# Optimization experiments

Hardware: AMD Instinct MI355X
Metric: run time of the kernel (lower is better)

## Reference

```python
import jax, jax.numpy as jnp
import numpy as np

# SLAY feature-map hyperparams (must match init_kwargs)
H, D, P, M, R = 4, 128, 16, 32, 2   # heads, head_dim, poly_dim, num_features, quad nodes
EPS = 1e-6
C = 2.0 + EPS
_nodes, _weights = np.polynomial.laguerre.laggauss(R)
QUAD_NODES = jnp.asarray(_nodes, jnp.float32) / C
QUAD_WEIGHTS = jnp.asarray(_weights, jnp.float32) / C

VOCAB, NUM_LABELS, EMBED_DIM = 100000, 32768, 512
B, S, K = 512, 64, 5


def slay_features(x, omega, anchors):
    """SLAY feature map: tensor product of anchored polynomial and PRF features.
    x: [N, EMBED_DIM] -> [N, R*H*P*M]"""
    N = x.shape[0]
    xr = x.reshape(N, H, D)
    xn = xr / jnp.clip(jnp.linalg.norm(xr, axis=-1, keepdims=True), 1e-6)  # safe_normalize
    # anchored polynomial features: [N, H, P]
    poly_feat = jnp.einsum('nhd,pd->nhp', xn, anchors) ** 2 / jnp.sqrt(float(P))
    # positive random features with Gauss-Laguerre quadrature: [R, N, H, M]
    prf_proj = jnp.einsum('nhd,rhdm->rnhm', xn, omega)
    s = QUAD_NODES.reshape(R, 1, 1, 1)
    sqrt_2s = jnp.sqrt(2.0 * jnp.clip(s, 0))
    prf_feat = jnp.exp(jnp.clip(prf_proj * sqrt_2s - s, -10.0, 10.0)) / jnp.sqrt(float(M))
    prf_feat = prf_feat * jnp.sqrt(jnp.clip(QUAD_WEIGHTS.reshape(R, 1, 1, 1), 0))
    # tensor-product fusion: [N, R, H, P, M] -> [N, R*H*P*M]
    fused = jnp.einsum('nhp,rnhm->nrhpm', poly_feat, prf_feat)
    return fused.reshape(N, -1)


def mean_embedding(indices, mask, embedding_table):
    embeds = embedding_table[indices]                       # [B, S, E]
    sum_embeds = jnp.sum(embeds * mask[:, :, None], axis=1)  # [B, E]
    sum_mask = jnp.sum(mask, axis=1, keepdims=True)
    return sum_embeds / jnp.clip(sum_mask, 1e-9)


def setup_inputs() -> dict:
    key = jax.random.key(0)
    k1, k2, k3, k4, k5, k6 = jax.random.split(key, 6)
    indices = jax.random.randint(k1, (B, S), 0, VOCAB)
    mask = jnp.ones((B, S), dtype=jnp.float32)
    labels = jax.random.randint(k2, (B, K), 0, NUM_LABELS)
    label_mask = jnp.ones((B, K), dtype=jnp.float32)
    embedding_table = jax.random.normal(k3, (VOCAB, EMBED_DIM), dtype=jnp.float32) * 0.02
    classifier_kernel = jax.random.normal(k4, (EMBED_DIM, NUM_LABELS), dtype=jnp.float32) * 0.02
    omega = jax.random.normal(k5, (R, H, D, M), dtype=jnp.float32)
    anchors = jax.random.normal(k6, (P, D), dtype=jnp.float32)
    anchors = anchors / jnp.linalg.norm(anchors, axis=-1, keepdims=True)
    return {"indices": indices, "mask": mask, "labels": labels, "label_mask": label_mask,
            "embedding_table": embedding_table, "classifier_kernel": classifier_kernel,
            "omega": omega, "anchors": anchors}


def reference(indices, mask, labels, label_mask, embedding_table, classifier_kernel, omega, anchors):
    query = mean_embedding(indices, mask, embedding_table)            # [B, E]
    phi_query = slay_features(query, omega, anchors)                  # [B, F]
    W_vecs = classifier_kernel.T                                      # [L, E]
    phi_W = slay_features(W_vecs, omega, anchors)                     # [L, F]  (dominant cost)
    Z_approx_vec = jnp.sum(phi_W, axis=0)                             # [F]
    denom = jnp.dot(phi_query, Z_approx_vec) + 1e-6                   # [B]
    log_Z = jnp.log(denom)
    safe_labels = jnp.maximum(labels, 0)
    W_pos = W_vecs[safe_labels]                                       # [B, K, E]
    phi_w_pos = slay_features(W_pos.reshape(-1, EMBED_DIM), omega, anchors).reshape(B, K, -1)
    nums = jnp.sum(phi_w_pos * phi_query[:, None, :], axis=-1) + 1e-6  # [B, K]
    log_probs = jnp.log(nums) - log_Z[:, None]
    loss_total = -jnp.sum(log_probs * label_mask)
    return loss_total / B
```

## Files before the change

### kernel.cpp

```cpp
#include <hip/hip_runtime.h>
#include <math.h>


namespace {
constexpr double Cq  = 2.0 + 1e-6;
constexpr double QN0 = 0.5857864376269049  / Cq;
constexpr double QN1 = 3.414213562373095   / Cq;
constexpr double QW0 = 0.8535533905932738  / Cq;
constexpr double QW1 = 0.14644660940672624 / Cq;

constexpr size_t OFF_POLYQ = 0;
constexpr size_t OFF_PRFQ  = 32768;
constexpr size_t OFF_Z     = OFF_PRFQ + 131072;
constexpr size_t OFF_ANCT  = OFF_Z + 4096;
constexpr size_t OFF_SLOT  = OFF_ANCT + 2048;
constexpr size_t OFF_FEAT  = OFF_SLOT + 32768;
constexpr size_t OFF_WPACK = OFF_FEAT + 819200;
constexpr size_t OFF_ZPART = OFF_WPACK + 43008;
}

__global__ void k_setup_a(const float* __restrict__ anchors,
                          const float* __restrict__ omega,
                          int* __restrict__ slot, float* __restrict__ Z,
                          float* __restrict__ out, float* __restrict__ anct,
                          float* __restrict__ Wpack)
{
    int t = blockIdx.x * 256 + threadIdx.x;
    for (int i = t; i < 32768; i += 16384) slot[i] = -1;
    if (t < 4096) Z[t] = 0.f;
    if (t == 0) out[0] = 0.f;
    if (t < 2048) {
        int p = t & 15, d = t >> 4;
        anct[t] = anchors[p * 128 + d];
    }
    for (int i = t; i < 4 * 128 * 84; i += 16384) {
        int o = i % 84, hd = i / 84, d = hd & 127, h = hd >> 7;
        float v = 0.f;
        if (o < 16) v = anchors[o * 128 + d];
        else if (o < 80) {
            int r = (o - 16) >> 5, m = (o - 16) & 31;
            v = omega[(((r * 4 + h) * 128) + d) * 32 + m];
        }
        Wpack[i] = v;
    }
}

__global__ void k_setup_b(const int* __restrict__ labels, int* __restrict__ slot)
{
    int i = blockIdx.x * 256 + threadIdx.x;
    if (i < 2560) slot[max(labels[i], 0)] = i;
}

__global__ void __launch_bounds__(256) k_embed_feat(const int* __restrict__ idx,
        const float* __restrict__ mask, const float* __restrict__ emb,
        const float* __restrict__ anct, const float* __restrict__ omega,
        float* __restrict__ polyq, float* __restrict__ prfq)
{
    __shared__ float xs[512];
    __shared__ float rnS[4];
    int b = blockIdx.x, t = threadIdx.x;

    float2 acc = make_float2(0.f, 0.f);
    float msum = 0.f;
#pragma unroll 8
    for (int s = 0; s < 64; ++s) {
        float mv = mask[b * 64 + s];
        const float2* row = (const float2*)(emb + (size_t)idx[b * 64 + s] * 512);
        float2 v = row[t];
        acc.x = fmaf(mv, v.x, acc.x);
        acc.y = fmaf(mv, v.y, acc.y);
        msum += mv;
    }
    float inv = 1.0f / fmaxf(msum, 1e-9f);
    xs[2 * t]     = acc.x * inv;
    xs[2 * t + 1] = acc.y * inv;
    __syncthreads();

    int w = t >> 6, lane = t & 63;
    {
        float v0 = xs[w * 128 + lane], v1 = xs[w * 128 + 64 + lane];
        float ss = fmaf(v0, v0, v1 * v1);
#pragma unroll
        for (int o = 1; o < 64; o <<= 1) ss += __shfl_xor(ss, o, 64);
        if (lane == 0) rnS[w] = 1.0f / fmaxf(sqrtf(ss), 1e-6f);
    }
    __syncthreads();

    const float s_[2] = {(float)QN0, (float)QN1};
    const float g_[2] = {sqrtf(2.0f * (float)QN0), sqrtf(2.0f * (float)QN1)};
    const float c_[2] = {sqrtf((float)QW0) * 0.17677669529663687f,
                         sqrtf((float)QW1) * 0.17677669529663687f};

    for (int tau = t; tau < 320; tau += 256) {
        int h = tau / 80, j = tau - h * 80;
        const float* xh = xs + h * 128;
        float a = 0.f;
        if (j < 16) {
            for (int d = 0; d < 128; ++d) a = fmaf(xh[d], anct[d * 16 + j], a);
            float v = a * rnS[h];
            polyq[(b * 4 + h) * 16 + j] = v * v * 0.25f;
        } else {
            int rj = j - 16, r = rj >> 5, m = rj & 31;
            const float* om = omega + ((size_t)(r * 4 + h) * 128) * 32 + m;
            for (int d = 0; d < 128; ++d) a = fmaf(xh[d], om[d * 32], a);
            float z = a * rnS[h] * g_[r] - s_[r];
            z = fminf(fmaxf(z, -10.f), 10.f);
            prfq[((b * 2 + r) * 4 + h) * 32 + m] = expf(z) * c_[r];
        }
    }
}

__global__ void __launch_bounds__(256) k_labels(const float* __restrict__ ck,
                                                const float* __restrict__ Wpack,
                                                const int* __restrict__ slot,
                                                float* __restrict__ feat,
                                                float* __restrict__ Zpart)
{
    __shared__ float xs[8192];
    __shared__ int slS[64];
    float* ex = xs;

    int t = threadIdx.x, w = t >> 6, lane = t & 63;
    int bid = blockIdx.x;
    int g = bid >> 2, h = bid & 3;
    int l0 = g * 64;

    if (t < 64) slS[t] = slot[l0 + t];

    {
        const float* src = ck + (size_t)h * 128 * 32768 + l0;
#pragma unroll
        for (int k = 0; k < 32; ++k) {
            int idx = k * 256 + t;
            int d = idx >> 6, lab = idx & 63;
            xs[idx] = src[(size_t)d * 32768 + lab];
        }
    }
    __syncthreads();

    int o0u = __builtin_amdgcn_readfirstlane(w * 21);
    const float* wrow = Wpack + (size_t)h * 128 * 84 + o0u;
    float acc[21] = {};
    float sumsq = 0.f;
    for (int d = 0; d < 128; ++d) {
        float xv = xs[d * 64 + lane];
        sumsq = fmaf(xv, xv, sumsq);
        const float* c = wrow + d * 84;
#pragma unroll
        for (int i = 0; i < 21; ++i) acc[i] = fmaf(xv, c[i], acc[i]);
    }
    __syncthreads();

#pragma unroll
    for (int i = 0; i < 21; ++i) {
        int o = o0u + i;
        if (o < 80) ex[lane * 85 + o] = acc[i];
    }
    if (w == 3) ex[lane * 85 + 80] = sumsq;
    __syncthreads();

    {
        int l = t & 63, part = t >> 6, o0 = part * 20;
        float rn = 1.0f / fmaxf(sqrtf(ex[l * 85 + 80]), 1e-6f);
        const float s_[2] = {(float)QN0, (float)QN1};
        const float g_[2] = {sqrtf(2.0f * (float)QN0), sqrtf(2.0f * (float)QN1)};
        const float c_[2] = {sqrtf((float)QW0) * 0.17677669529663687f,
                             sqrtf((float)QW1) * 0.17677669529663687f};
#pragma unroll
        for (int i = 0; i < 20; ++i) {
            int o = o0 + i;
            float v = ex[l * 85 + o];
            if (o < 16) {
                v = v * rn;
                v = v * v * 0.25f;
            } else {
                int r = (o - 16) >> 5;
                float z = v * rn * g_[r] - s_[r];
                z = fminf(fmaxf(z, -10.f), 10.f);
                v = expf(z) * c_[r];
            }
            ex[l * 85 + o] = v;
        }
    }
    __syncthreads();

    for (int j = 0; j < 64; ++j) {
        int s = slS[j];
        if (s >= 0 && t < 80)
            feat[((size_t)s * 4 + h) * 80 + t] = ex[j * 85 + t];
    }

    if (t < 128) {
        int r = t >> 6, p0 = ((t >> 3) & 7) * 2, m0 = (t & 7) * 4;
        float z0[4] = {}, z1[4] = {};
        for (int j = 0; j < 64; ++j) {
            const float* row = ex + j * 85;
            float pa = row[p0], pb = row[p0 + 1];
            const float* pf = row + 16 + r * 32 + m0;
#pragma unroll
            for (int k = 0; k < 4; ++k) {
                float fv = pf[k];
                z0[k] = fmaf(pa, fv, z0[k]);
                z1[k] = fmaf(pb, fv, z1[k]);
            }
        }
        float* zp = Zpart + (size_t)bid * 1024;
#pragma unroll
        for (int k = 0; k < 4; ++k) {
            zp[(r * 16 + p0) * 32 + m0 + k]     = z0[k];
            zp[(r * 16 + p0 + 1) * 32 + m0 + k] = z1[k];
        }
    }
}

__global__ void k_zreduce(const float* __restrict__ Zpart, float* __restrict__ Z)
{
    int tid = blockIdx.x * 256 + threadIdx.x;
    int e = tid & 1023, h = (tid >> 10) & 3, chunk = tid >> 12;
    float sum = 0.f;
    int g0 = chunk * 64;
#pragma unroll 4
    for (int g = g0; g < g0 + 64; ++g)
        sum += Zpart[(size_t)((g << 2) | h) * 1024 + e];
    atomicAdd(&Z[(e >> 9) * 2048 + h * 512 + (e & 511)], sum);
}

__global__ void k_final(const float* __restrict__ polyq, const float* __restrict__ prfq,
                        const float* __restrict__ Z, const int* __restrict__ labels,
                        const float* __restrict__ lmask, const int* __restrict__ slot,
                        const float* __restrict__ feat, float* __restrict__ out)
{
    int t = threadIdx.x, lane = t & 63;
    int b = blockIdx.x * 4 + (t >> 6);

    float acc = 0.f;
    for (int i = 0; i < 64; ++i) {
        int f = i * 64 + lane;
        int m = f & 31, p = (f >> 5) & 15, hh = (f >> 9) & 3, r = f >> 11;
        float phi = polyq[(b * 4 + hh) * 16 + p] * prfq[((b * 2 + r) * 4 + hh) * 32 + m];
        acc = fmaf(phi, Z[f], acc);
    }
#pragma unroll
    for (int o = 1; o < 64; o <<= 1) acc += __shfl_xor(acc, o, 64);
    float logZb = logf(acc + 1e-6f);

    if (lane < 20) {
        int k = lane >> 2, h = lane & 3;
        int l = max(labels[b * 5 + k], 0);
        int s = slot[l];
        const float4* f4 = (const float4*)(feat + ((size_t)s * 4 + h) * 80);
        const float* pq = polyq + (b * 4 + h) * 16;
        const float* q0 = prfq + ((b * 2 + 0) * 4 + h) * 32;
        const float* q1 = prfq + ((b * 2 + 1) * 4 + h) * 32;

        float pd = 0.f;
#pragma unroll
        for (int j = 0; j < 4; ++j) {
            float4 fp = f4[j];
            pd = fmaf(fp.x, pq[4*j+0], pd);
            pd = fmaf(fp.y, pq[4*j+1], pd);
            pd = fmaf(fp.z, pq[4*j+2], pd);
            pd = fmaf(fp.w, pq[4*j+3], pd);
        }
        float f0 = 0.f, f1 = 0.f;
#pragma unroll
        for (int j = 0; j < 8; ++j) {
            float4 fv = f4[4 + j];
            f0 = fmaf(fv.x, q0[4*j+0], f0);
            f0 = fmaf(fv.y, q0[4*j+1], f0);
            f0 = fmaf(fv.z, q0[4*j+2], f0);
            f0 = fmaf(fv.w, q0[4*j+3], f0);
            float4 fw = f4[12 + j];
            f1 = fmaf(fw.x, q1[4*j+0], f1);
            f1 = fmaf(fw.y, q1[4*j+1], f1);
            f1 = fmaf(fw.z, q1[4*j+2], f1);
            f1 = fmaf(fw.w, q1[4*j+3], f1);
        }
        float c = pd * (f0 + f1);
        c += __shfl_xor(c, 1, 64);
        c += __shfl_xor(c, 2, 64);
        if (h == 0) {
            float val = (logf(c + 1e-6f) - logZb) * lmask[b * 5 + k];
            atomicAdd(out, val * (-1.0f / 512.0f));
        }
    }
}

extern "C" void kernel_launch(void* const* d_in, const int* in_sizes, int n_in,
                              void* d_out, int out_size, void* d_ws, size_t ws_size,
                              hipStream_t stream)
{
    const int*   indices = (const int*)  d_in[0];
    const float* mask    = (const float*)d_in[1];
    const int*   labels  = (const int*)  d_in[2];
    const float* lmask   = (const float*)d_in[3];
    const float* emb     = (const float*)d_in[4];
    const float* ck      = (const float*)d_in[5];
    const float* omega   = (const float*)d_in[6];
    const float* anchors = (const float*)d_in[7];
    float* ws  = (float*)d_ws;
    float* out = (float*)d_out;
    int*   slot = (int*)(ws + OFF_SLOT);

    k_setup_a<<<64, 256, 0, stream>>>(anchors, omega, slot, ws + OFF_Z, out,
                                      ws + OFF_ANCT, ws + OFF_WPACK);
    k_setup_b<<<10, 256, 0, stream>>>(labels, slot);
    k_embed_feat<<<512, 256, 0, stream>>>(indices, mask, emb, ws + OFF_ANCT, omega,
                                          ws + OFF_POLYQ, ws + OFF_PRFQ);
    k_labels<<<2048, 256, 0, stream>>>(ck, ws + OFF_WPACK, slot,
                                       ws + OFF_FEAT, ws + OFF_ZPART);
    k_zreduce<<<128, 256, 0, stream>>>(ws + OFF_ZPART, ws + OFF_Z);
    k_final<<<128, 256, 0, stream>>>(ws + OFF_POLYQ, ws + OFF_PRFQ, ws + OFF_Z,
                                     labels, lmask, slot, ws + OFF_FEAT, out);
}
```

Baseline: 396.5 us.

## Fuse pipeline into cooperative persistent megakernel with atomic tile scheduler

Replaces the separate embed, label-feature, Z-reduce and final kernels with one cooperative kernel of 1024 persistent blocks. The blocks pull label tiles from an atomic counter and separate the phases with grid syncs. The label-slot indirection is dropped: features are now stored for every label and indexed directly. The Wpack layout is padded to 24 floats per row so the weights can be read with float4 loads. This removes launch gaps and the slot setup but writes a much larger feature buffer, and falls back to three launches if the cooperative launch fails.

```diff
diff --git a/kernel.cpp b/kernel.cpp
--- a/kernel.cpp
+++ b/kernel.cpp
@@ -1,5 +1,8 @@
 #include <hip/hip_runtime.h>
+#include <hip/hip_cooperative_groups.h>
 #include <math.h>
+
+namespace cg = cooperative_groups;
 
 
 namespace {
@@ -13,275 +16,294 @@
 constexpr size_t OFF_PRFQ  = 32768;
 constexpr size_t OFF_Z     = OFF_PRFQ + 131072;
 constexpr size_t OFF_ANCT  = OFF_Z + 4096;
-constexpr size_t OFF_SLOT  = OFF_ANCT + 2048;
-constexpr size_t OFF_FEAT  = OFF_SLOT + 32768;
-constexpr size_t OFF_WPACK = OFF_FEAT + 819200;
-constexpr size_t OFF_ZPART = OFF_WPACK + 43008;
+constexpr size_t OFF_CTR   = OFF_ANCT + 2048;
+constexpr size_t OFF_WPACK = OFF_CTR + 16;
+constexpr size_t OFF_ZPART = OFF_WPACK + 49152;
+constexpr size_t OFF_FEAT  = OFF_ZPART + 2097152;
 }
 
-__global__ void k_setup_a(const float* __restrict__ anchors,
-                          const float* __restrict__ omega,
-                          int* __restrict__ slot, float* __restrict__ Z,
-                          float* __restrict__ out, float* __restrict__ anct,
-                          float* __restrict__ Wpack)
+__global__ void k_setup(const float* __restrict__ anchors,
+                        const float* __restrict__ omega,
+                        float* __restrict__ Z, float* __restrict__ out,
+                        float* __restrict__ anct, int* __restrict__ ctr,
+                        float* __restrict__ Wpack)
 {
     int t = blockIdx.x * 256 + threadIdx.x;
-    for (int i = t; i < 32768; i += 16384) slot[i] = -1;
     if (t < 4096) Z[t] = 0.f;
-    if (t == 0) out[0] = 0.f;
+    if (t == 0) { out[0] = 0.f; ctr[0] = 0; }
     if (t < 2048) {
         int p = t & 15, d = t >> 4;
         anct[t] = anchors[p * 128 + d];
     }
-    for (int i = t; i < 4 * 128 * 84; i += 16384) {
-        int o = i % 84, hd = i / 84, d = hd & 127, h = hd >> 7;
+    for (int i = t; i < 4 * 4 * 128 * 24; i += 16384) {
+        int iw = i % 24;
+        int hwd = i / 24;
+        int d = hwd & 127;
+        int hw = hwd >> 7;
+        int w = hw & 3, h = hw >> 2;
+        int o = w * 21 + iw;
         float v = 0.f;
-        if (o < 16) v = anchors[o * 128 + d];
-        else if (o < 80) {
-            int r = (o - 16) >> 5, m = (o - 16) & 31;
-            v = omega[(((r * 4 + h) * 128) + d) * 32 + m];
+        if (iw < 21 && o < 80) {
+            if (o < 16) v = anchors[o * 128 + d];
+            else {
+                int r = (o - 16) >> 5, m = (o - 16) & 31;
+                v = omega[(((r * 4 + h) * 128) + d) * 32 + m];
+            }
         }
         Wpack[i] = v;
     }
 }
 
-__global__ void k_setup_b(const int* __restrict__ labels, int* __restrict__ slot)
+template<int MODE>
+__global__ void __launch_bounds__(256, 4)
+k_mega(const int* __restrict__ idx, const float* __restrict__ mask,
+       const int* __restrict__ labels, const float* __restrict__ lmask,
+       const float* __restrict__ emb, const float* __restrict__ ck,
+       const float* __restrict__ omega, const float* __restrict__ anct,
+       const float* __restrict__ Wpack, int* __restrict__ ctr,
+       float* __restrict__ polyq, float* __restrict__ prfq,
+       float* __restrict__ Z, float* __restrict__ Zpart,
+       float* __restrict__ feat, float* __restrict__ out)
 {
-    int i = blockIdx.x * 256 + threadIdx.x;
-    if (i < 2560) slot[max(labels[i], 0)] = i;
-}
-
-__global__ void __launch_bounds__(256) k_embed_feat(const int* __restrict__ idx,
-        const float* __restrict__ mask, const float* __restrict__ emb,
-        const float* __restrict__ anct, const float* __restrict__ omega,
-        float* __restrict__ polyq, float* __restrict__ prfq)
-{
-    __shared__ float xs[512];
+    __shared__ float smem[8192];
     __shared__ float rnS[4];
-    int b = blockIdx.x, t = threadIdx.x;
-
-    float2 acc = make_float2(0.f, 0.f);
-    float msum = 0.f;
-#pragma unroll 8
-    for (int s = 0; s < 64; ++s) {
-        float mv = mask[b * 64 + s];
-        const float2* row = (const float2*)(emb + (size_t)idx[b * 64 + s] * 512);
-        float2 v = row[t];
-        acc.x = fmaf(mv, v.x, acc.x);
-        acc.y = fmaf(mv, v.y, acc.y);
-        msum += mv;
-    }
-    float inv = 1.0f / fmaxf(msum, 1e-9f);
-    xs[2 * t]     = acc.x * inv;
-    xs[2 * t + 1] = acc.y * inv;
-    __syncthreads();
-
-    int w = t >> 6, lane = t & 63;
-    {
-        float v0 = xs[w * 128 + lane], v1 = xs[w * 128 + 64 + lane];
-        float ss = fmaf(v0, v0, v1 * v1);
-#pragma unroll
-        for (int o = 1; o < 64; o <<= 1) ss += __shfl_xor(ss, o, 64);
-        if (lane == 0) rnS[w] = 1.0f / fmaxf(sqrtf(ss), 1e-6f);
-    }
-    __syncthreads();
+    __shared__ int   sTile;
+
+    int t = threadIdx.x;
+    int lane = t & 63;
+    int w = t >> 6;
 
     const float s_[2] = {(float)QN0, (float)QN1};
     const float g_[2] = {sqrtf(2.0f * (float)QN0), sqrtf(2.0f * (float)QN1)};
     const float c_[2] = {sqrtf((float)QW0) * 0.17677669529663687f,
                          sqrtf((float)QW1) * 0.17677669529663687f};
 
-    for (int tau = t; tau < 320; tau += 256) {
-        int h = tau / 80, j = tau - h * 80;
-        const float* xh = xs + h * 128;
-        float a = 0.f;
-        if (j < 16) {
-            for (int d = 0; d < 128; ++d) a = fmaf(xh[d], anct[d * 16 + j], a);
-            float v = a * rnS[h];
-            polyq[(b * 4 + h) * 16 + j] = v * v * 0.25f;
-        } else {
-            int rj = j - 16, r = rj >> 5, m = rj & 31;
-            const float* om = omega + ((size_t)(r * 4 + h) * 128) * 32 + m;
-            for (int d = 0; d < 128; ++d) a = fmaf(xh[d], om[d * 32], a);
-            float z = a * rnS[h] * g_[r] - s_[r];
-            z = fminf(fmaxf(z, -10.f), 10.f);
-            prfq[((b * 2 + r) * 4 + h) * 32 + m] = expf(z) * c_[r];
-        }
-    }
-}
-
-__global__ void __launch_bounds__(256) k_labels(const float* __restrict__ ck,
-                                                const float* __restrict__ Wpack,
-                                                const int* __restrict__ slot,
-                                                float* __restrict__ feat,
-                                                float* __restrict__ Zpart)
-{
-    __shared__ float xs[8192];
-    __shared__ int slS[64];
-    float* ex = xs;
-
-    int t = threadIdx.x, w = t >> 6, lane = t & 63;
-    int bid = blockIdx.x;
-    int g = bid >> 2, h = bid & 3;
-    int l0 = g * 64;
-
-    if (t < 64) slS[t] = slot[l0 + t];
-
-    {
-        const float* src = ck + (size_t)h * 128 * 32768 + l0;
-#pragma unroll
-        for (int k = 0; k < 32; ++k) {
-            int idx = k * 256 + t;
-            int d = idx >> 6, lab = idx & 63;
-            xs[idx] = src[(size_t)d * 32768 + lab];
-        }
-    }
-    __syncthreads();
-
-    int o0u = __builtin_amdgcn_readfirstlane(w * 21);
-    const float* wrow = Wpack + (size_t)h * 128 * 84 + o0u;
-    float acc[21] = {};
-    float sumsq = 0.f;
-    for (int d = 0; d < 128; ++d) {
-        float xv = xs[d * 64 + lane];
-        sumsq = fmaf(xv, xv, sumsq);
-        const float* c = wrow + d * 84;
-#pragma unroll
-        for (int i = 0; i < 21; ++i) acc[i] = fmaf(xv, c[i], acc[i]);
-    }
-    __syncthreads();
-
-#pragma unroll
-    for (int i = 0; i < 21; ++i) {
-        int o = o0u + i;
-        if (o < 80) ex[lane * 85 + o] = acc[i];
-    }
-    if (w == 3) ex[lane * 85 + 80] = sumsq;
-    __syncthreads();
-
-    {
-        int l = t & 63, part = t >> 6, o0 = part * 20;
-        float rn = 1.0f / fmaxf(sqrtf(ex[l * 85 + 80]), 1e-6f);
-        const float s_[2] = {(float)QN0, (float)QN1};
-        const float g_[2] = {sqrtf(2.0f * (float)QN0), sqrtf(2.0f * (float)QN1)};
-        const float c_[2] = {sqrtf((float)QW0) * 0.17677669529663687f,
-                             sqrtf((float)QW1) * 0.17677669529663687f};
-#pragma unroll
-        for (int i = 0; i < 20; ++i) {
-            int o = o0 + i;
-            float v = ex[l * 85 + o];
-            if (o < 16) {
-                v = v * rn;
-                v = v * v * 0.25f;
-            } else {
-                int r = (o - 16) >> 5;
-                float z = v * rn * g_[r] - s_[r];
-                z = fminf(fmaxf(z, -10.f), 10.f);
-                v = expf(z) * c_[r];
-            }
-            ex[l * 85 + o] = v;
-        }
-    }
-    __syncthreads();
-
-    for (int j = 0; j < 64; ++j) {
-        int s = slS[j];
-        if (s >= 0 && t < 80)
-            feat[((size_t)s * 4 + h) * 80 + t] = ex[j * 85 + t];
-    }
-
-    if (t < 128) {
-        int r = t >> 6, p0 = ((t >> 3) & 7) * 2, m0 = (t & 7) * 4;
-        float z0[4] = {}, z1[4] = {};
-        for (int j = 0; j < 64; ++j) {
-            const float* row = ex + j * 85;
-            float pa = row[p0], pb = row[p0 + 1];
-            const float* pf = row + 16 + r * 32 + m0;
-#pragma unroll
-            for (int k = 0; k < 4; ++k) {
-                float fv = pf[k];
-                z0[k] = fmaf(pa, fv, z0[k]);
-                z1[k] = fmaf(pb, fv, z1[k]);
-            }
-        }
-        float* zp = Zpart + (size_t)bid * 1024;
-#pragma unroll
-        for (int k = 0; k < 4; ++k) {
-            zp[(r * 16 + p0) * 32 + m0 + k]     = z0[k];
-            zp[(r * 16 + p0 + 1) * 32 + m0 + k] = z1[k];
-        }
-    }
-}
-
-__global__ void k_zreduce(const float* __restrict__ Zpart, float* __restrict__ Z)
-{
-    int tid = blockIdx.x * 256 + threadIdx.x;
-    int e = tid & 1023, h = (tid >> 10) & 3, chunk = tid >> 12;
-    float sum = 0.f;
-    int g0 = chunk * 64;
+    if (MODE == 0 || MODE == 1) {
+        if (blockIdx.x < 512) {
+            int b = blockIdx.x;
+            float2 acc = make_float2(0.f, 0.f);
+            float msum = 0.f;
+#pragma unroll 8
+            for (int s = 0; s < 64; ++s) {
+                float mv = mask[b * 64 + s];
+                const float2* row = (const float2*)(emb + (size_t)idx[b * 64 + s] * 512);
+                float2 v = row[t];
+                acc.x = fmaf(mv, v.x, acc.x);
+                acc.y = fmaf(mv, v.y, acc.y);
+                msum += mv;
+            }
+            float inv = 1.0f / fmaxf(msum, 1e-9f);
+            smem[2 * t]     = acc.x * inv;
+            smem[2 * t + 1] = acc.y * inv;
+            __syncthreads();
+            {
+                float v0 = smem[w * 128 + lane], v1 = smem[w * 128 + 64 + lane];
+                float ss = fmaf(v0, v0, v1 * v1);
+#pragma unroll
+                for (int o = 1; o < 64; o <<= 1) ss += __shfl_xor(ss, o, 64);
+                if (lane == 0) rnS[w] = 1.0f / fmaxf(sqrtf(ss), 1e-6f);
+            }
+            __syncthreads();
+            for (int tau = t; tau < 320; tau += 256) {
+                int h = tau / 80, j = tau - h * 80;
+                const float* xh = smem + h * 128;
+                if (j < 16) {
+                    float a = 0.f;
+                    for (int d = 0; d < 128; ++d) a = fmaf(xh[d], anct[d * 16 + j], a);
+                    float v = a * rnS[h];
+                    polyq[(b * 4 + h) * 16 + j] = v * v * 0.25f;
+                } else {
+                    int rj = j - 16, r = rj >> 5, m = rj & 31;
+                    const float* om = omega + ((size_t)(r * 4 + h) * 128) * 32 + m;
+                    float a = 0.f;
+                    for (int d = 0; d < 128; ++d) a = fmaf(xh[d], om[d * 32], a);
+                    float z = a * rnS[h] * g_[r] - s_[r];
+                    z = fminf(fmaxf(z, -10.f), 10.f);
+                    prfq[((b * 2 + r) * 4 + h) * 32 + m] = expf(z) * c_[r];
+                }
+            }
+            __syncthreads();
+        }
+
+        int wu = __builtin_amdgcn_readfirstlane(w);
+        while (true) {
+            if (t == 0) sTile = atomicAdd(ctr, 1);
+            __syncthreads();
+            int tile = sTile;
+            if (tile >= 2048) break;
+            int g = tile >> 2, h = tile & 3;
+            int l0 = g << 6;
+
+            {
+                const float* src = ck + (size_t)h * 128 * 32768 + l0;
+#pragma unroll
+                for (int k2 = 0; k2 < 32; ++k2) {
+                    int ix = k2 * 256 + t;
+                    int d = ix >> 6, lab = ix & 63;
+                    smem[ix] = src[(size_t)d * 32768 + lab];
+                }
+            }
+            __syncthreads();
+
+            const float* wv = Wpack + ((size_t)(h * 4 + wu) * 128) * 24;
+            float acc[21] = {};
+            float sumsq = 0.f;
+            for (int d = 0; d < 128; ++d) {
+                float xv = smem[d * 64 + lane];
+                sumsq = fmaf(xv, xv, sumsq);
+                const float* c = wv + d * 24;
+                float4 c0 = *(const float4*)(c);
+                float4 c1 = *(const float4*)(c + 4);
+                float4 c2 = *(const float4*)(c + 8);
+                float4 c3 = *(const float4*)(c + 12);
+                float4 c4 = *(const float4*)(c + 16);
+                float cl = c[20];
+                acc[0]  = fmaf(xv, c0.x, acc[0]);  acc[1]  = fmaf(xv, c0.y, acc[1]);
+                acc[2]  = fmaf(xv, c0.z, acc[2]);  acc[3]  = fmaf(xv, c0.w, acc[3]);
+                acc[4]  = fmaf(xv, c1.x, acc[4]);  acc[5]  = fmaf(xv, c1.y, acc[5]);
+                acc[6]  = fmaf(xv, c1.z, acc[6]);  acc[7]  = fmaf(xv, c1.w, acc[7]);
+                acc[8]  = fmaf(xv, c2.x, acc[8]);  acc[9]  = fmaf(xv, c2.y, acc[9]);
+                acc[10] = fmaf(xv, c2.z, acc[10]); acc[11] = fmaf(xv, c2.w, acc[11]);
+                acc[12] = fmaf(xv, c3.x, acc[12]); acc[13] = fmaf(xv, c3.y, acc[13]);
+                acc[14] = fmaf(xv, c3.z, acc[14]); acc[15] = fmaf(xv, c3.w, acc[15]);
+                acc[16] = fmaf(xv, c4.x, acc[16]); acc[17] = fmaf(xv, c4.y, acc[17]);
+                acc[18] = fmaf(xv, c4.z, acc[18]); acc[19] = fmaf(xv, c4.w, acc[19]);
+                acc[20] = fmaf(xv, cl,   acc[20]);
+            }
+            __syncthreads();
+
+            int o0 = wu * 21;
+#pragma unroll
+            for (int i = 0; i < 21; ++i) {
+                int o = o0 + i;
+                if (o < 80) smem[lane * 85 + o] = acc[i];
+            }
+            if (wu == 3) smem[lane * 85 + 80] = sumsq;
+            __syncthreads();
+
+            {
+                int l = t & 63, part = t >> 6, of = part * 20;
+                float rn = 1.0f / fmaxf(sqrtf(smem[l * 85 + 80]), 1e-6f);
+#pragma unroll
+                for (int i = 0; i < 20; ++i) {
+                    int o = of + i;
+                    float v = smem[l * 85 + o];
+                    if (o < 16) {
+                        v = v * rn;
+                        v = v * v * 0.25f;
+                    } else {
+                        int r = (o - 16) >> 5;
+                        float z = v * rn * g_[r] - s_[r];
+                        z = fminf(fmaxf(z, -10.f), 10.f);
+                        v = expf(z) * c_[r];
+                    }
+                    smem[l * 85 + o] = v;
+                }
+            }
+            __syncthreads();
+
+            for (int e = t; e < 5120; e += 256) {
+                int j = e / 80, o = e - j * 80;
+                feat[((size_t)(l0 + j) * 4 + h) * 80 + o] = smem[j * 85 + o];
+            }
+
+            if (t < 128) {
+                int r = t >> 6, p0 = ((t >> 3) & 7) * 2, m0 = (t & 7) * 4;
+                float z0[4] = {}, z1[4] = {};
+                for (int j = 0; j < 64; ++j) {
+                    const float* row = smem + j * 85;
+                    float pa = row[p0], pb = row[p0 + 1];
+                    const float* pf = row + 16 + r * 32 + m0;
+#pragma unroll
+                    for (int k2 = 0; k2 < 4; ++k2) {
+                        float fv = pf[k2];
+                        z0[k2] = fmaf(pa, fv, z0[k2]);
+                        z1[k2] = fmaf(pb, fv, z1[k2]);
+                    }
+                }
+                float* zp = Zpart + (size_t)tile * 1024;
+#pragma unroll
+                for (int k2 = 0; k2 < 4; ++k2) {
+                    zp[(r * 16 + p0) * 32 + m0 + k2]     = z0[k2];
+                    zp[(r * 16 + p0 + 1) * 32 + m0 + k2] = z1[k2];
+                }
+            }
+            __syncthreads();
+        }
+    }
+
+    if (MODE == 0) cg::this_grid().sync();
+
+    if (MODE == 0 || MODE == 2) {
+        if (blockIdx.x < 128) {
+            int tid = blockIdx.x * 256 + t;
+            int e = tid & 1023, h = (tid >> 10) & 3, chunk = tid >> 12;
+            float sum = 0.f;
+            int g0 = chunk * 64;
 #pragma unroll 4
-    for (int g = g0; g < g0 + 64; ++g)
-        sum += Zpart[(size_t)((g << 2) | h) * 1024 + e];
-    atomicAdd(&Z[(e >> 9) * 2048 + h * 512 + (e & 511)], sum);
-}
-
-__global__ void k_final(const float* __restrict__ polyq, const float* __restrict__ prfq,
-                        const float* __restrict__ Z, const int* __restrict__ labels,
-                        const float* __restrict__ lmask, const int* __restrict__ slot,
-                        const float* __restrict__ feat, float* __restrict__ out)
-{
-    int t = threadIdx.x, lane = t & 63;
-    int b = blockIdx.x * 4 + (t >> 6);
-
-    float acc = 0.f;
-    for (int i = 0; i < 64; ++i) {
-        int f = i * 64 + lane;
-        int m = f & 31, p = (f >> 5) & 15, hh = (f >> 9) & 3, r = f >> 11;
-        float phi = polyq[(b * 4 + hh) * 16 + p] * prfq[((b * 2 + r) * 4 + hh) * 32 + m];
-        acc = fmaf(phi, Z[f], acc);
-    }
-#pragma unroll
-    for (int o = 1; o < 64; o <<= 1) acc += __shfl_xor(acc, o, 64);
-    float logZb = logf(acc + 1e-6f);
-
-    if (lane < 20) {
-        int k = lane >> 2, h = lane & 3;
-        int l = max(labels[b * 5 + k], 0);
-        int s = slot[l];
-        const float4* f4 = (const float4*)(feat + ((size_t)s * 4 + h) * 80);
-        const float* pq = polyq + (b * 4 + h) * 16;
-        const float* q0 = prfq + ((b * 2 + 0) * 4 + h) * 32;
-        const float* q1 = prfq + ((b * 2 + 1) * 4 + h) * 32;
-
-        float pd = 0.f;
-#pragma unroll
-        for (int j = 0; j < 4; ++j) {
-            float4 fp = f4[j];
-            pd = fmaf(fp.x, pq[4*j+0], pd);
-            pd = fmaf(fp.y, pq[4*j+1], pd);
-            pd = fmaf(fp.z, pq[4*j+2], pd);
-            pd = fmaf(fp.w, pq[4*j+3], pd);
-        }
-        float f0 = 0.f, f1 = 0.f;
-#pragma unroll
-        for (int j = 0; j < 8; ++j) {
-            float4 fv = f4[4 + j];
-            f0 = fmaf(fv.x, q0[4*j+0], f0);
-            f0 = fmaf(fv.y, q0[4*j+1], f0);
-            f0 = fmaf(fv.z, q0[4*j+2], f0);
-            f0 = fmaf(fv.w, q0[4*j+3], f0);
-            float4 fw = f4[12 + j];
-            f1 = fmaf(fw.x, q1[4*j+0], f1);
-            f1 = fmaf(fw.y, q1[4*j+1], f1);
-            f1 = fmaf(fw.z, q1[4*j+2], f1);
-            f1 = fmaf(fw.w, q1[4*j+3], f1);
-        }
-        float c = pd * (f0 + f1);
-        c += __shfl_xor(c, 1, 64);
-        c += __shfl_xor(c, 2, 64);
-        if (h == 0) {
-            float val = (logf(c + 1e-6f) - logZb) * lmask[b * 5 + k];
-            atomicAdd(out, val * (-1.0f / 512.0f));
+            for (int g = g0; g < g0 + 64; ++g)
+                sum += Zpart[(size_t)((g << 2) | h) * 1024 + e];
+            atomicAdd(&Z[(e >> 9) * 2048 + h * 512 + (e & 511)], sum);
+        }
+    }
+
+    if (MODE == 0) cg::this_grid().sync();
+
+    if (MODE == 0 || MODE == 3) {
+        if (blockIdx.x < 128) {
+            int b = blockIdx.x * 4 + w;
+
+            float acc = 0.f;
+            for (int i = 0; i < 64; ++i) {
+                int f = i * 64 + lane;
+                int m = f & 31, p = (f >> 5) & 15, hh = (f >> 9) & 3, r = f >> 11;
+                float phi = polyq[(b * 4 + hh) * 16 + p] *
+                            prfq[((b * 2 + r) * 4 + hh) * 32 + m];
+                acc = fmaf(phi, Z[f], acc);
+            }
+#pragma unroll
+            for (int o = 1; o < 64; o <<= 1) acc += __shfl_xor(acc, o, 64);
+            float logZb = logf(acc + 1e-6f);
+
+            if (lane < 20) {
+                int k = lane >> 2, h = lane & 3;
+                int l = max(labels[b * 5 + k], 0);
+                const float4* f4 = (const float4*)(feat + ((size_t)l * 4 + h) * 80);
+                const float* pq = polyq + (b * 4 + h) * 16;
+                const float* q0 = prfq + ((b * 2 + 0) * 4 + h) * 32;
+                const float* q1 = prfq + ((b * 2 + 1) * 4 + h) * 32;
+
+                float pd = 0.f;
+#pragma unroll
+                for (int j = 0; j < 4; ++j) {
+                    float4 fp = f4[j];
+                    pd = fmaf(fp.x, pq[4*j+0], pd);
+                    pd = fmaf(fp.y, pq[4*j+1], pd);
+                    pd = fmaf(fp.z, pq[4*j+2], pd);
+                    pd = fmaf(fp.w, pq[4*j+3], pd);
+                }
+                float f0 = 0.f, f1 = 0.f;
+#pragma unroll
+                for (int j = 0; j < 8; ++j) {
+                    float4 fv = f4[4 + j];
+                    f0 = fmaf(fv.x, q0[4*j+0], f0);
+                    f0 = fmaf(fv.y, q0[4*j+1], f0);
+                    f0 = fmaf(fv.z, q0[4*j+2], f0);
+                    f0 = fmaf(fv.w, q0[4*j+3], f0);
+                    float4 fw = f4[12 + j];
+                    f1 = fmaf(fw.x, q1[4*j+0], f1);
+                    f1 = fmaf(fw.y, q1[4*j+1], f1);
+                    f1 = fmaf(fw.z, q1[4*j+2], f1);
+                    f1 = fmaf(fw.w, q1[4*j+3], f1);
+                }
+                float c = pd * (f0 + f1);
+                c += __shfl_xor(c, 1, 64);
+                c += __shfl_xor(c, 2, 64);
+                if (h == 0) {
+                    float val = (logf(c + 1e-6f) - logZb) * lmask[b * 5 + k];
+                    atomicAdd(out, val * (-1.0f / 512.0f));
+                }
+            }
         }
     }
 }
@@ -300,16 +322,40 @@
     const float* anchors = (const float*)d_in[7];
     float* ws  = (float*)d_ws;
     float* out = (float*)d_out;
-    int*   slot = (int*)(ws + OFF_SLOT);
-
-    k_setup_a<<<64, 256, 0, stream>>>(anchors, omega, slot, ws + OFF_Z, out,
-                                      ws + OFF_ANCT, ws + OFF_WPACK);
-    k_setup_b<<<10, 256, 0, stream>>>(labels, slot);
-    k_embed_feat<<<512, 256, 0, stream>>>(indices, mask, emb, ws + OFF_ANCT, omega,
-                                          ws + OFF_POLYQ, ws + OFF_PRFQ);
-    k_labels<<<2048, 256, 0, stream>>>(ck, ws + OFF_WPACK, slot,
-                                       ws + OFF_FEAT, ws + OFF_ZPART);
-    k_zreduce<<<128, 256, 0, stream>>>(ws + OFF_ZPART, ws + OFF_Z);
-    k_final<<<128, 256, 0, stream>>>(ws + OFF_POLYQ, ws + OFF_PRFQ, ws + OFF_Z,
-                                     labels, lmask, slot, ws + OFF_FEAT, out);
+
+    float* polyq = ws + OFF_POLYQ;
+    float* prfq  = ws + OFF_PRFQ;
+    float* Zp    = ws + OFF_Z;
+    float* anct  = ws + OFF_ANCT;
+    int*   ctr   = (int*)(ws + OFF_CTR);
+    float* Wpack = ws + OFF_WPACK;
+    float* Zpart = ws + OFF_ZPART;
+    float* feat  = ws + OFF_FEAT;
+
+    k_setup<<<64, 256, 0, stream>>>(anchors, omega, Zp, out, anct, ctr, Wpack);
+
+    const int*   a_idx   = indices;  const float* a_mask = mask;
+    const int*   a_lab   = labels;   const float* a_lm   = lmask;
+    const float* a_emb   = emb;      const float* a_ck   = ck;
+    const float* a_om    = omega;    const float* a_anct = anct;
+    const float* a_wp    = Wpack;    int*         a_ctr  = ctr;
+    float* a_pq = polyq; float* a_pr = prfq; float* a_z = Zp;
+    float* a_zp = Zpart; float* a_ft = feat; float* a_out = out;
+    void* args[] = { &a_idx, &a_mask, &a_lab, &a_lm, &a_emb, &a_ck, &a_om,
+                     &a_anct, &a_wp, &a_ctr, &a_pq, &a_pr, &a_z, &a_zp,
+                     &a_ft, &a_out };
+
+    hipError_t e = hipLaunchCooperativeKernel(
+        reinterpret_cast<void*>(&k_mega<0>), dim3(1024), dim3(256),
+        args, 0, stream);
+
+    if (e != hipSuccess) {
+        (void)hipGetLastError();
+        k_mega<1><<<1024, 256, 0, stream>>>(indices, mask, labels, lmask, emb,
+            ck, omega, anct, Wpack, ctr, polyq, prfq, Zp, Zpart, feat, out);
+        k_mega<2><<<128, 256, 0, stream>>>(indices, mask, labels, lmask, emb,
+            ck, omega, anct, Wpack, ctr, polyq, prfq, Zp, Zpart, feat, out);
+        k_mega<3><<<128, 256, 0, stream>>>(indices, mask, labels, lmask, emb,
+            ck, omega, anct, Wpack, ctr, polyq, prfq, Zp, Zpart, feat, out);
+    }
 }
```

Result: slower. 634.4 us (+60.0%).
